# Performance work log

Measured on AMD Instinct MI355X. Metric: run time of the kernel, lower is better.

Reference implementation:

```python
import jax, jax.numpy as jnp
import numpy as np

B = 1024      # batchsz
T = 80        # max_review_len
E = 100       # embedding_len
U = 256       # units
V = 10000     # total_words


def _lstm_cell(x, c, h, wf, bf, wi, bi, wc, bc, wo, bo):
    # Faithful to LSTMlayer.call: four separate concat+matmul+bias gates.
    hx = jnp.concatenate([h, x], axis=1)          # [B, U + sec_dim]
    gf = jax.nn.sigmoid(hx @ wf + bf)             # forget gate
    gi = jax.nn.sigmoid(hx @ wi + bi)             # input gate (gr / wr1)
    ct = jnp.tanh(hx @ wc + bc)                   # candidate (wr2)
    c_new = gf * c + gi * ct
    go = jax.nn.sigmoid(hx @ wo + bo)             # output gate
    h_new = go * jnp.tanh(c_new)
    return c_new, h_new


def setup_inputs() -> dict:
    key = jax.random.key(0)
    ks = jax.random.split(key, 21)
    inp = {"tokens": jax.random.randint(ks[0], (B, T), 0, V, dtype=jnp.int32)}
    inp["emb"] = jax.random.normal(ks[1], (V, E), dtype=jnp.float32) * 0.1
    # Layer 1: sec_dim = E; Layer 2: sec_dim = U. stddev=0.1 matches init_weights.
    names = ["wf1", "wi1", "wc1", "wo1", "wf2", "wi2", "wc2", "wo2"]
    dims = [U + E] * 4 + [U + U] * 4
    for i, (n, d) in enumerate(zip(names, dims)):
        inp[n] = jax.random.normal(ks[2 + i], (d, U), dtype=jnp.float32) * 0.1
        inp["b" + n[1:]] = jnp.zeros((U,), dtype=jnp.float32)
    inp["w_out"] = jax.random.normal(ks[10], (U, 1), dtype=jnp.float32) * 0.1
    inp["b_out"] = jnp.zeros((1,), dtype=jnp.float32)
    return inp


def reference(tokens, emb, wf1, bf1, wi1, bi1, wc1, bc1, wo1, bo1,
              wf2, bf2, wi2, bi2, wc2, bc2, wo2, bo2, w_out, b_out):
    x = emb[tokens]                               # [B, T, E]
    init = (jnp.zeros((B, U), x.dtype), jnp.zeros((B, U), x.dtype),
            jnp.zeros((B, U), x.dtype), jnp.zeros((B, U), x.dtype))

    def step(carry, xt):
        c1, h1, c2, h2 = carry
        c1, h1 = _lstm_cell(xt, c1, h1, wf1, bf1, wi1, bi1, wc1, bc1, wo1, bo1)
        c2, h2 = _lstm_cell(h1, c2, h2, wf2, bf2, wi2, bi2, wc2, bc2, wo2, bo2)
        return (c1, h1, c2, h2), None

    carry, _ = jax.lax.scan(step, init, jnp.swapaxes(x, 0, 1))  # scan over T
    h2_last = carry[3]                            # [B, U]
    return jax.nn.sigmoid(h2_last @ w_out + b_out)  # [B, 1]
```

## Files before the change

### kernel.cpp

```cpp
#include <hip/hip_runtime.h>

typedef unsigned short u16;
typedef unsigned int uint;

using f32x4 = __attribute__((ext_vector_type(4))) float;
using bf16x8 = __attribute__((ext_vector_type(8))) __bf16;
using u32x4 = __attribute__((ext_vector_type(4))) uint;

static __device__ __forceinline__ bf16x8 as_bf16x8(uint4 u) {
    union { uint4 a; bf16x8 b; } c; c.a = u; return c.b;
}
static __device__ __forceinline__ bf16x8 as_bf16x8v(u32x4 u) {
    union { u32x4 a; bf16x8 b; } c; c.a = u; return c.b;
}
static __device__ __forceinline__ float bf2f(u16 h) {
    union { uint u; float f; } c; c.u = ((uint)h) << 16; return c.f;
}
static __device__ __forceinline__ u16 f2bf(float f) {
    union { float f; uint u; } c; c.f = f;
    uint u = c.u;
    return (u16)((u + 0x7fffu + ((u >> 16) & 1u)) >> 16);
}
static __device__ __forceinline__ float fast_sigmoid(float x) {
    x = fminf(30.f, fmaxf(-30.f, x));
    return __builtin_amdgcn_rcpf(1.0f + __builtin_amdgcn_exp2f(x * -1.44269504f));
}
static __device__ __forceinline__ float fast_tanh(float x) {
    x = fminf(15.f, fmaxf(-15.f, x));
    return 1.0f - 2.0f * __builtin_amdgcn_rcpf(1.0f + __builtin_amdgcn_exp2f(x * 2.88539008f));
}

static __device__ __forceinline__ u32x4 load_b128_sc0(const u16* p) {
    u32x4 r;
    asm volatile("global_load_dwordx4 %0, %1, off sc0" : "=v"(r) : "v"(p) : "memory");
    return r;
}
static __device__ __forceinline__ void wait_vm0_fence_sched() {
    asm volatile("s_waitcnt vmcnt(0)" ::: "memory");
    __builtin_amdgcn_sched_barrier(0);
}

static __device__ __forceinline__ float vext(f32x4 v, int i) {
    float r = v[0];
    r = (i == 1) ? v[1] : r;
    r = (i == 2) ? v[2] : r;
    r = (i == 3) ? v[3] : r;
    return r;
}
static __device__ __forceinline__ float sel4(float a0, float a1, float a2, float a3, int i) {
    float r = a0;
    r = (i == 1) ? a1 : r;
    r = (i == 2) ? a2 : r;
    r = (i == 3) ? a3 : r;
    return r;
}

static __device__ __forceinline__ int detect_fp32(const uint* w, int nwords) {
    int hits = 0;
    for (int i = 0; i < nwords; ++i) { uint e = (w[i] >> 7) & 0xffu; hits += (e >= 0x80u); }
    return hits > (nwords >> 3);
}
static __device__ __forceinline__ u16 load_bf(const void* p, int i, int fp32) {
    return fp32 ? f2bf(((const float*)p)[i]) : ((const u16*)p)[i];
}

__global__ void pack_w(const void* wf, const void* wi, const void* wc, const void* wo,
                       const void* bbf, const void* bbi, const void* bbc, const void* bbo,
                       u16* __restrict__ wp, u16* __restrict__ bp, int K, int KSTEPS) {
    __shared__ int sfp;
    if (threadIdx.x == 0) sfp = detect_fp32((const uint*)wf, 256);
    __syncthreads();
    const int fp32 = sfp;
    int w = blockIdx.x / KSTEPS, ks = blockIdx.x % KSTEPS;
    int nt = threadIdx.x >> 6, lane = threadIdx.x & 63;
    int c16 = lane & 15, q = lane >> 4;
    int n = w * 64 + nt * 16 + c16;
    int u = n >> 2, g = n & 3;
    const void* W = (g == 0) ? wf : (g == 1) ? wi : (g == 2) ? wc : wo;
    union { u16 v[8]; uint4 u4; } tmp;
#pragma unroll
    for (int j = 0; j < 8; ++j) {
        int k = ks * 32 + q * 8 + j;
        tmp.v[j] = (k < K) ? load_bf(W, k * 256 + u, fp32) : (u16)0;
    }
    *(uint4*)(wp + ((w * KSTEPS + ks) * 4 + nt) * 512 + lane * 8) = tmp.u4;
    if (ks == 0 && threadIdx.x < 64) {
        int n2 = w * 64 + threadIdx.x;
        int g2 = n2 & 3;
        const void* B = (g2 == 0) ? bbf : (g2 == 1) ? bbi : (g2 == 2) ? bbc : bbo;
        bp[n2] = load_bf(B, n2 >> 2, fp32);
    }
}

__global__ void pack_misc(const void* emb, const void* w_out, const void* b_out,
                          u16* __restrict__ embp, u16* __restrict__ wob,
                          u16* __restrict__ bob, uint* __restrict__ hzero) {
    __shared__ int sfp;
    if (threadIdx.x == 0) sfp = detect_fp32((const uint*)emb, 256);
    __syncthreads();
    const int fp32 = sfp;
    int gid = blockIdx.x * blockDim.x + threadIdx.x;
    int stride = gridDim.x * blockDim.x;
    for (int i = gid; i < 1000000; i += stride)
        embp[i] = load_bf(emb, i, fp32);
    for (int i = gid; i < 526336; i += stride) hzero[i] = 0;
    if (blockIdx.x == 0) {
        __shared__ int sfp2;
        if (threadIdx.x == 0) sfp2 = detect_fp32((const uint*)w_out, 128);
        __syncthreads();
        if (threadIdx.x < 256) wob[threadIdx.x] = load_bf(w_out, threadIdx.x, sfp2);
        if (threadIdx.x == 0) bob[0] = load_bf(b_out, 0, sfp2);
    }
}

static __device__ __forceinline__ void wv_wait(uint* grp, uint phase, int lane) {
    const uint* fp = grp + (lane & 15);
    uint* cnt = grp + 32;
    int k = 0;
    while (true) {
        uint v;
        asm volatile("global_load_dword %0, %1, off sc0\n\t"
                     "s_waitcnt vmcnt(0)"
                     : "=v"(v) : "v"(fp) : "memory");
        if (__all((int)(v >= phase))) break;
        __builtin_amdgcn_s_sleep(2);
        if (((++k) & 7) == 0 &&
            __hip_atomic_load(cnt, __ATOMIC_RELAXED,
                              __HIP_MEMORY_SCOPE_AGENT) >= 16u * phase)
            break;
    }
}

static __device__ __forceinline__ void wv_arrive(uint* ldsc_ch, uint* grp, int g,
                                                 uint phase, int lane) {
    asm volatile("s_waitcnt vmcnt(0)" ::: "memory");
    if (lane == 0) {
        uint old = __hip_atomic_fetch_add(ldsc_ch, 1u, __ATOMIC_RELAXED,
                                          __HIP_MEMORY_SCOPE_WORKGROUP);
        if (old == 8u * phase - 1u) {
            uint* slot = grp + g;
            asm volatile("global_store_dword %0, %1, off sc0"
                         :: "v"(slot), "v"(phase) : "memory");
            __hip_atomic_fetch_add(grp + 32, 1u, __ATOMIC_RELAXED,
                                   __HIP_MEMORY_SCOPE_AGENT);
        }
    }
}

#define CSLAB 16384

__global__ void __launch_bounds__(1024, 1)
lstm_kernel(const int* __restrict__ tokens, const u16* __restrict__ embp,
            const u16* __restrict__ wp1, const u16* __restrict__ b1p,
            const u16* __restrict__ wp2, const u16* __restrict__ b2p,
            const u16* __restrict__ wob, const u16* __restrict__ bob,
            u16* __restrict__ h1g, u16* __restrict__ h2g,
            uint* __restrict__ flags, float* __restrict__ out) {
    __shared__ __align__(16) u16 w1s[12 * 4 * 512];
    __shared__ __align__(16) u16 w2s[16 * 4 * 512];
    __shared__ uint ldsc[2];
    __shared__ __align__(16) float outscr[1024];

    const int tid = threadIdx.x;
    const int bid = blockIdx.x;
    const int r2 = bid & 7;
    const int g = bid >> 3;
    const int lane = tid & 63;
    const int wv = tid >> 6;
    const int half = wv >> 3;
    const int w8 = wv & 7;
    const int nt = w8 & 3;
    const int mb = (w8 >> 2) * 2;
    const int c16 = lane & 15, q = lane >> 4;

    const int b = lane & 3;
    const int ulz = nt * 4 + ((lane & 15) >> 2);
    const int gunit = g * 16 + ulz;

    {
        const uint4* s1 = (const uint4*)(wp1 + g * (12 * 4 * 512));
        uint4* d1 = (uint4*)w1s;
        for (int i = tid; i < 3072; i += 1024) d1[i] = s1[i];
        const uint4* s2 = (const uint4*)(wp2 + g * (16 * 4 * 512));
        uint4* d2 = (uint4*)w2s;
        for (int i = tid; i < 4096; i += 1024) d2[i] = s2[i];
        if (tid < 2) ldsc[tid] = 0u;
    }
    ushort4 bl1 = *(const ushort4*)(b1p + gunit * 4);
    ushort4 bl2 = *(const ushort4*)(b2p + gunit * 4);
    const float b1f = bf2f(bl1.x), b1i = bf2f(bl1.y), b1c = bf2f(bl1.z), b1o = bf2f(bl1.w);
    const float b2f = bf2f(bl2.x), b2i = bf2f(bl2.y), b2c = bf2f(bl2.z), b2o = bf2f(bl2.w);
    float c1a = 0.f, c1b = 0.f, c2a = 0.f, c2b = 0.f;
    uint* fg = flags + (half * 8 + r2) * 64;
    uint* lc = &ldsc[half];
    __syncthreads();

    const u16* bp1 = w1s + nt * 512 + lane * 8;
    const u16* bp2 = w2s + nt * 512 + lane * 8;

    ushort4 xlo[4], xhi[4];
#define LOAD_X(m, t)                                                           \
    {                                                                          \
        int row = r2 * 128 + half * 64 + (m) * 16 + c16;                       \
        int tok = tokens[row * 80 + (t)];                                      \
        const u16* xb = embp + tok * 100 + q * 8;                              \
        _Pragma("unroll")                                                      \
        for (int k2 = 0; k2 < 4; ++k2) {                                       \
            xlo[k2] = *(const ushort4*)(xb + k2 * 32);                         \
            xhi[k2] = *(const ushort4*)(xb + k2 * 32 + 4);                     \
        }                                                                      \
    }
#define XFRAG(k2) ({ union { ushort4 a[2]; bf16x8 v; } xu;                     \
                     xu.a[0] = xlo[k2]; xu.a[1] = xhi[k2]; xu.v; })

#define GATES(accv, B0, B1, B2, B3, cref, hout)                                \
    {                                                                          \
        float v0 = vext(accv, b);                                              \
        float v1 = __shfl_xor(vext(accv, b ^ 1), 1, 64);                       \
        float v2 = __shfl_xor(vext(accv, b ^ 2), 2, 64);                       \
        float v3 = __shfl_xor(vext(accv, b ^ 3), 3, 64);                       \
        float zf = sel4(v0, v1, v2, v3, b);                                    \
        float zi = sel4(v0, v1, v2, v3, b ^ 1);                                \
        float zc = sel4(v0, v1, v2, v3, b ^ 2);                                \
        float zo = sel4(v0, v1, v2, v3, b ^ 3);                                \
        float gf = fast_sigmoid(zf + B0);                                      \
        float gi = fast_sigmoid(zi + B1);                                      \
        float gc = fast_tanh(zc + B2);                                         \
        float go = fast_sigmoid(zo + B3);                                      \
        float cn = gf * cref + gi * gc;                                        \
        cref = cn;                                                             \
        hout = f2bf(go * fast_tanh(cn));                                       \
    }

#define MSUB(m, acc1, c1ref, c2ref, p2r, p1r, p2w, p1w)                        \
    {                                                                          \
        const int loffm = (q >> 1) * 1024 + ((m) * 16 + c16) * 16 + (q & 1) * 8; \
        const int hidxm = g * 1024 + ((m) * 16 + q * 4 + b) * 16 + ulz;        \
        const u16* h2b = h2g + (((p2r) * 2 + half) * 8 + r2) * CSLAB + loffm;  \
        const u16* h1b = h1g + (((p1r) * 2 + half) * 8 + r2) * CSLAB + loffm;  \
        u32x4 ag2[8], ag1[8];                                                  \
        _Pragma("unroll")                                                      \
        for (int ks = 0; ks < 8; ++ks) ag2[ks] = load_b128_sc0(h2b + ks * 2048); \
        _Pragma("unroll")                                                      \
        for (int ks = 0; ks < 8; ++ks) ag1[ks] = load_b128_sc0(h1b + ks * 2048); \
        wait_vm0_fence_sched();                                                \
        f32x4 acc2 = (f32x4){0.f, 0.f, 0.f, 0.f};                              \
        _Pragma("unroll")                                                      \
        for (int ks = 0; ks < 8; ++ks)                                         \
            acc2 = __builtin_amdgcn_mfma_f32_16x16x32_bf16(                    \
                as_bf16x8v(ag2[ks]), as_bf16x8(*(const uint4*)(bp2 + ks * 2048)), acc2, 0, 0, 0); \
        _Pragma("unroll")                                                      \
        for (int ks = 0; ks < 8; ++ks)                                         \
            acc2 = __builtin_amdgcn_mfma_f32_16x16x32_bf16(                    \
                as_bf16x8v(ag1[ks]), as_bf16x8(*(const uint4*)(bp2 + (8 + ks) * 2048)), acc2, 0, 0, 0); \
        _Pragma("unroll")                                                      \
        for (int ks = 0; ks < 8; ++ks)                                         \
            acc1 = __builtin_amdgcn_mfma_f32_16x16x32_bf16(                    \
                as_bf16x8v(ag1[ks]), as_bf16x8(*(const uint4*)(bp1 + ks * 2048)), acc1, 0, 0, 0); \
        u16 h2o, h1o;                                                          \
        GATES(acc2, b2f, b2i, b2c, b2o, c2ref, h2o);                           \
        GATES(acc1, b1f, b1i, b1c, b1o, c1ref, h1o);                           \
        h2g[(((p2w) * 2 + half) * 8 + r2) * CSLAB + hidxm] = h2o;              \
        h1g[(((p1w) * 2 + half) * 8 + r2) * CSLAB + hidxm] = h1o;              \
    }

    {
        LOAD_X(mb, 0);
        f32x4 acc = (f32x4){0.f, 0.f, 0.f, 0.f};
#pragma unroll
        for (int k2 = 0; k2 < 4; ++k2)
            acc = __builtin_amdgcn_mfma_f32_16x16x32_bf16(
                XFRAG(k2), as_bf16x8(*(const uint4*)(bp1 + (8 + k2) * 2048)), acc, 0, 0, 0);
        u16 h1o;
        GATES(acc, b1f, b1i, b1c, b1o, c1a, h1o);
        h1g[((0 * 2 + half) * 8 + r2) * CSLAB + g * 1024 + (mb * 16 + q * 4 + b) * 16 + ulz] = h1o;
        LOAD_X(mb + 1, 0);
        f32x4 accB = (f32x4){0.f, 0.f, 0.f, 0.f};
#pragma unroll
        for (int k2 = 0; k2 < 4; ++k2)
            accB = __builtin_amdgcn_mfma_f32_16x16x32_bf16(
                XFRAG(k2), as_bf16x8(*(const uint4*)(bp1 + (8 + k2) * 2048)), accB, 0, 0, 0);
        u16 h1oB;
        GATES(accB, b1f, b1i, b1c, b1o, c1b, h1oB);
        h1g[((0 * 2 + half) * 8 + r2) * CSLAB + g * 1024 + ((mb + 1) * 16 + q * 4 + b) * 16 + ulz] = h1oB;
        wv_arrive(lc, fg, g, 1u, lane);
    }

#pragma unroll 1
    for (int i = 0; i < 79; ++i) {
        const int p_h2r = (i + 1) & 1, p_h1r = i & 1;
        const int p_h2w = i & 1, p_h1w = (i + 1) & 1;

        LOAD_X(mb, i + 1);
        f32x4 acc1a = (f32x4){0.f, 0.f, 0.f, 0.f};
#pragma unroll
        for (int k2 = 0; k2 < 4; ++k2)
            acc1a = __builtin_amdgcn_mfma_f32_16x16x32_bf16(
                XFRAG(k2), as_bf16x8(*(const uint4*)(bp1 + (8 + k2) * 2048)), acc1a, 0, 0, 0);
        LOAD_X(mb + 1, i + 1);
        f32x4 acc1b = (f32x4){0.f, 0.f, 0.f, 0.f};
#pragma unroll
        for (int k2 = 0; k2 < 4; ++k2)
            acc1b = __builtin_amdgcn_mfma_f32_16x16x32_bf16(
                XFRAG(k2), as_bf16x8(*(const uint4*)(bp1 + (8 + k2) * 2048)), acc1b, 0, 0, 0);

        wv_wait(fg, (uint)(i + 1), lane);

        __builtin_amdgcn_s_setprio(1);
        MSUB(mb, acc1a, c1a, c2a, p_h2r, p_h1r, p_h2w, p_h1w);
        MSUB(mb + 1, acc1b, c1b, c2b, p_h2r, p_h1r, p_h2w, p_h1w);
        __builtin_amdgcn_s_setprio(0);

        wv_arrive(lc, fg, g, (uint)(i + 2), lane);
    }

    {
        wv_wait(fg, 80u, lane);
#pragma unroll 1
        for (int s = 0; s < 2; ++s) {
            const int m = mb + s;
            const int loffm = (q >> 1) * 1024 + (m * 16 + c16) * 16 + (q & 1) * 8;
            const int hidxm = g * 1024 + (m * 16 + q * 4 + b) * 16 + ulz;
            const u16* h2b = h2g + ((0 * 2 + half) * 8 + r2) * CSLAB + loffm;
            const u16* h1b = h1g + ((1 * 2 + half) * 8 + r2) * CSLAB + loffm;
            u32x4 ag2[8], ag1[8];
#pragma unroll
            for (int ks = 0; ks < 8; ++ks) ag2[ks] = load_b128_sc0(h2b + ks * 2048);
#pragma unroll
            for (int ks = 0; ks < 8; ++ks) ag1[ks] = load_b128_sc0(h1b + ks * 2048);
            wait_vm0_fence_sched();
            f32x4 acc2 = (f32x4){0.f, 0.f, 0.f, 0.f};
#pragma unroll
            for (int ks = 0; ks < 8; ++ks)
                acc2 = __builtin_amdgcn_mfma_f32_16x16x32_bf16(
                    as_bf16x8v(ag2[ks]), as_bf16x8(*(const uint4*)(bp2 + ks * 2048)), acc2, 0, 0, 0);
#pragma unroll
            for (int ks = 0; ks < 8; ++ks)
                acc2 = __builtin_amdgcn_mfma_f32_16x16x32_bf16(
                    as_bf16x8v(ag1[ks]), as_bf16x8(*(const uint4*)(bp2 + (8 + ks) * 2048)), acc2, 0, 0, 0);
            u16 h2o;
            if (s == 0) { GATES(acc2, b2f, b2i, b2c, b2o, c2a, h2o); }
            else        { GATES(acc2, b2f, b2i, b2c, b2o, c2b, h2o); }
            h2g[((1 * 2 + half) * 8 + r2) * CSLAB + hidxm] = h2o;
        }
        wv_arrive(lc, fg, g, 81u, lane);
        wv_wait(fg, 81u, lane);
    }
    __syncthreads();

    if (g == 0) {
#pragma unroll 1
        for (int ch = 0; ch < 2; ++ch) {
            const u16* base = h2g + ((1 * 2 + ch) * 8 + r2) * CSLAB;
            int rr = tid >> 4, s = tid & 15;
            const u16* hp = base + s * 1024 + rr * 16;
            u32x4 hv0 = load_b128_sc0(hp);
            u32x4 hv1 = load_b128_sc0(hp + 8);
            wait_vm0_fence_sched();
            const u16* wq = wob + s * 16;
            union { u32x4 v[2]; u16 h[16]; } hu; hu.v[0] = hv0; hu.v[1] = hv1;
            float dot = 0.f;
#pragma unroll
            for (int k = 0; k < 16; ++k) dot += bf2f(hu.h[k]) * bf2f(wq[k]);
            __syncthreads();
            outscr[rr * 16 + s] = dot;
            __syncthreads();
            if (tid < 64) {
                float ssum = 0.f;
                for (int k = 0; k < 16; ++k) ssum += outscr[tid * 16 + k];
                out[r2 * 128 + ch * 64 + tid] = fast_sigmoid(ssum + bf2f(bob[0]));
            }
        }
    }
}

extern "C" void kernel_launch(void* const* d_in, const int* in_sizes, int n_in,
                              void* d_out, int out_size, void* d_ws, size_t ws_size,
                              hipStream_t stream) {
    const int* tokens = (const int*)d_in[0];
    const void* emb = d_in[1];
    const void* wf1 = d_in[2];  const void* bf1_ = d_in[3];
    const void* wi1 = d_in[4];  const void* bi1_ = d_in[5];
    const void* wc1 = d_in[6];  const void* bc1_ = d_in[7];
    const void* wo1 = d_in[8];  const void* bo1_ = d_in[9];
    const void* wf2 = d_in[10]; const void* bf2_ = d_in[11];
    const void* wi2 = d_in[12]; const void* bi2_ = d_in[13];
    const void* wc2 = d_in[14]; const void* bc2_ = d_in[15];
    const void* wo2 = d_in[16]; const void* bo2_ = d_in[17];
    const void* w_out = d_in[18];
    const void* b_out = d_in[19];

    u16* wp1 = (u16*)d_ws;
    u16* wp2 = wp1 + 16 * 12 * 4 * 512;
    u16* b1p = wp2 + 16 * 16 * 4 * 512;
    u16* b2p = b1p + 1024;
    u16* wob = b2p + 1024;
    u16* bob = wob + 256;
    u16* embp = bob + 8;
    u16* h1g = embp + 1000000;
    u16* h2g = h1g + 524288;
    uint* flags = (uint*)(h2g + 524288);

    pack_w<<<dim3(16 * 12), dim3(256), 0, stream>>>(wf1, wi1, wc1, wo1, bf1_, bi1_, bc1_, bo1_,
                                                    wp1, b1p, 356, 12);
    pack_w<<<dim3(16 * 16), dim3(256), 0, stream>>>(wf2, wi2, wc2, wo2, bf2_, bi2_, bc2_, bo2_,
                                                    wp2, b2p, 512, 16);
    pack_misc<<<dim3(512), dim3(256), 0, stream>>>(emb, w_out, b_out, embp, wob, bob, (uint*)h1g);
    lstm_kernel<<<dim3(128), dim3(1024), 0, stream>>>(tokens, embp, wp1, b1p, wp2, b2p,
                                                      wob, bob, h1g, h2g, flags, (float*)d_out);
}
```

Measured before the change: 782.0 us.

## Replace global barrier wait with per-fragment readiness polling and pipelined K-loop

Instead of waiting for all producer groups to finish a timestep before loading hidden state, each wave polls per-group flags and waits only for the K-slice it needs next. It starts at a staggered slice offset (gp) so consumers fan out across producers. Loads for the next slice are double-buffered against the MFMAs of the current one, and the two M-subtiles are interleaved. This aims to overlap cross-block synchronization latency with compute, at the cost of more flag polling traffic and a more complex ordering that depends on flag semantics.

```diff
diff --git a/kernel.cpp b/kernel.cpp
--- a/kernel.cpp
+++ b/kernel.cpp
@@ -165,6 +165,7 @@
     const int bid = blockIdx.x;
     const int r2 = bid & 7;
     const int g = bid >> 3;
+    const int gp = g >> 1;
     const int lane = tid & 63;
     const int wv = tid >> 6;
     const int half = wv >> 3;
@@ -232,36 +233,57 @@
         hout = f2bf(go * fast_tanh(cn));                                       \
     }
 
-#define MSUB(m, acc1, c1ref, c2ref, p2r, p1r, p2w, p1w)                        \
+#define FRAG_WAIT(ksp, ph)                                                     \
+    if (((rmask >> (2 * (ksp))) & 3u) != 3u) {                                 \
+        const uint* fpp = fg + (lane & 15);                                    \
+        uint* cntp = fg + 32;                                                  \
+        int kk = 0;                                                            \
+        while (true) {                                                         \
+            uint v;                                                            \
+            asm volatile("global_load_dword %0, %1, off sc0\n\t"               \
+                         "s_waitcnt vmcnt(0)"                                  \
+                         : "=v"(v) : "v"(fpp) : "memory");                     \
+            unsigned long long bl = __ballot((int)(v >= (ph)));                \
+            rmask = (uint)(bl & 0xffffull);                                    \
+            if (((rmask >> (2 * (ksp))) & 3u) == 3u) break;                    \
+            __builtin_amdgcn_s_sleep(1);                                       \
+            if (((++kk) & 15) == 0 &&                                          \
+                __hip_atomic_load(cntp, __ATOMIC_RELAXED,                      \
+                                  __HIP_MEMORY_SCOPE_AGENT) >= 16u * (ph)) {   \
+                rmask = 0xffffu;                                               \
+                break;                                                         \
+            }                                                                  \
+        }                                                                      \
+    }
+
+#define FRAG_STEP(J)                                                           \
     {                                                                          \
-        const int loffm = (q >> 1) * 1024 + ((m) * 16 + c16) * 16 + (q & 1) * 8; \
-        const int hidxm = g * 1024 + ((m) * 16 + q * 4 + b) * 16 + ulz;        \
-        const u16* h2b = h2g + (((p2r) * 2 + half) * 8 + r2) * CSLAB + loffm;  \
-        const u16* h1b = h1g + (((p1r) * 2 + half) * 8 + r2) * CSLAB + loffm;  \
-        u32x4 ag2[8], ag1[8];                                                  \
-        _Pragma("unroll")                                                      \
-        for (int ks = 0; ks < 8; ++ks) ag2[ks] = load_b128_sc0(h2b + ks * 2048); \
-        _Pragma("unroll")                                                      \
-        for (int ks = 0; ks < 8; ++ks) ag1[ks] = load_b128_sc0(h1b + ks * 2048); \
-        wait_vm0_fence_sched();                                                \
-        f32x4 acc2 = (f32x4){0.f, 0.f, 0.f, 0.f};                              \
-        _Pragma("unroll")                                                      \
-        for (int ks = 0; ks < 8; ++ks)                                         \
-            acc2 = __builtin_amdgcn_mfma_f32_16x16x32_bf16(                    \
-                as_bf16x8v(ag2[ks]), as_bf16x8(*(const uint4*)(bp2 + ks * 2048)), acc2, 0, 0, 0); \
-        _Pragma("unroll")                                                      \
-        for (int ks = 0; ks < 8; ++ks)                                         \
-            acc2 = __builtin_amdgcn_mfma_f32_16x16x32_bf16(                    \
-                as_bf16x8v(ag1[ks]), as_bf16x8(*(const uint4*)(bp2 + (8 + ks) * 2048)), acc2, 0, 0, 0); \
-        _Pragma("unroll")                                                      \
-        for (int ks = 0; ks < 8; ++ks)                                         \
-            acc1 = __builtin_amdgcn_mfma_f32_16x16x32_bf16(                    \
-                as_bf16x8v(ag1[ks]), as_bf16x8(*(const uint4*)(bp1 + ks * 2048)), acc1, 0, 0, 0); \
-        u16 h2o, h1o;                                                          \
-        GATES(acc2, b2f, b2i, b2c, b2o, c2ref, h2o);                           \
-        GATES(acc1, b1f, b1i, b1c, b1o, c1ref, h1o);                           \
-        h2g[(((p2w) * 2 + half) * 8 + r2) * CSLAB + hidxm] = h2o;              \
-        h1g[(((p1w) * 2 + half) * 8 + r2) * CSLAB + hidxm] = h1o;              \
+        u32x4 n2a = f2a, n1a = f1a, n2b = f2b, n1b = f1b;                      \
+        if ((J) < 7) {                                                         \
+            int kspn = (gp + (J) + 1) & 7;                                     \
+            FRAG_WAIT(kspn, phase);                                            \
+            const u16* h2fn = h2base + kspn * 2048;                            \
+            const u16* h1fn = h1base + kspn * 2048;                            \
+            n2a = load_b128_sc0(h2fn + loffA);                                 \
+            n1a = load_b128_sc0(h1fn + loffA);                                 \
+            n2b = load_b128_sc0(h2fn + loffB);                                 \
+            n1b = load_b128_sc0(h1fn + loffB);                                 \
+            asm volatile("s_waitcnt vmcnt(4)" ::: "memory");                   \
+        } else {                                                               \
+            asm volatile("s_waitcnt vmcnt(0)" ::: "memory");                   \
+        }                                                                      \
+        __builtin_amdgcn_sched_barrier(0);                                     \
+        int kspc = (gp + (J)) & 7;                                             \
+        const uint4 w2lo = *(const uint4*)(bp2 + kspc * 2048);                 \
+        const uint4 w2hi = *(const uint4*)(bp2 + (8 + kspc) * 2048);           \
+        const uint4 w1lo = *(const uint4*)(bp1 + kspc * 2048);                 \
+        acc2a = __builtin_amdgcn_mfma_f32_16x16x32_bf16(as_bf16x8v(f2a), as_bf16x8(w2lo), acc2a, 0, 0, 0); \
+        acc1a = __builtin_amdgcn_mfma_f32_16x16x32_bf16(as_bf16x8v(f1a), as_bf16x8(w1lo), acc1a, 0, 0, 0); \
+        acc2a = __builtin_amdgcn_mfma_f32_16x16x32_bf16(as_bf16x8v(f1a), as_bf16x8(w2hi), acc2a, 0, 0, 0); \
+        acc2b = __builtin_amdgcn_mfma_f32_16x16x32_bf16(as_bf16x8v(f2b), as_bf16x8(w2lo), acc2b, 0, 0, 0); \
+        acc1b = __builtin_amdgcn_mfma_f32_16x16x32_bf16(as_bf16x8v(f1b), as_bf16x8(w1lo), acc1b, 0, 0, 0); \
+        acc2b = __builtin_amdgcn_mfma_f32_16x16x32_bf16(as_bf16x8v(f1b), as_bf16x8(w2hi), acc2b, 0, 0, 0); \
+        f2a = n2a; f1a = n1a; f2b = n2b; f1b = n1b;                            \
     }
 
     {
@@ -304,11 +326,38 @@
             acc1b = __builtin_amdgcn_mfma_f32_16x16x32_bf16(
                 XFRAG(k2), as_bf16x8(*(const uint4*)(bp1 + (8 + k2) * 2048)), acc1b, 0, 0, 0);
 
-        wv_wait(fg, (uint)(i + 1), lane);
+        const uint phase = (uint)(i + 1);
+        const u16* h2base = h2g + ((p_h2r * 2 + half) * 8 + r2) * CSLAB;
+        const u16* h1base = h1g + ((p_h1r * 2 + half) * 8 + r2) * CSLAB;
+        const int loffA = (q >> 1) * 1024 + (mb * 16 + c16) * 16 + (q & 1) * 8;
+        const int loffB = loffA + 256;
+        f32x4 acc2a = (f32x4){0.f, 0.f, 0.f, 0.f};
+        f32x4 acc2b = (f32x4){0.f, 0.f, 0.f, 0.f};
+        uint rmask = 0u;
+
+        FRAG_WAIT(gp, phase);
+        const u16* h2f0 = h2base + gp * 2048;
+        const u16* h1f0 = h1base + gp * 2048;
+        u32x4 f2a = load_b128_sc0(h2f0 + loffA);
+        u32x4 f1a = load_b128_sc0(h1f0 + loffA);
+        u32x4 f2b = load_b128_sc0(h2f0 + loffB);
+        u32x4 f1b = load_b128_sc0(h1f0 + loffB);
 
         __builtin_amdgcn_s_setprio(1);
-        MSUB(mb, acc1a, c1a, c2a, p_h2r, p_h1r, p_h2w, p_h1w);
-        MSUB(mb + 1, acc1b, c1b, c2b, p_h2r, p_h1r, p_h2w, p_h1w);
+        FRAG_STEP(0) FRAG_STEP(1) FRAG_STEP(2) FRAG_STEP(3)
+        FRAG_STEP(4) FRAG_STEP(5) FRAG_STEP(6) FRAG_STEP(7)
+
+        u16 h2oA, h1oA, h2oB, h1oB;
+        GATES(acc2a, b2f, b2i, b2c, b2o, c2a, h2oA);
+        GATES(acc1a, b1f, b1i, b1c, b1o, c1a, h1oA);
+        GATES(acc2b, b2f, b2i, b2c, b2o, c2b, h2oB);
+        GATES(acc1b, b1f, b1i, b1c, b1o, c1b, h1oB);
+        const int hidxA = g * 1024 + (mb * 16 + q * 4 + b) * 16 + ulz;
+        const int hidxB = hidxA + 256;
+        h2g[((p_h2w * 2 + half) * 8 + r2) * CSLAB + hidxA] = h2oA;
+        h1g[((p_h1w * 2 + half) * 8 + r2) * CSLAB + hidxA] = h1oA;
+        h2g[((p_h2w * 2 + half) * 8 + r2) * CSLAB + hidxB] = h2oB;
+        h1g[((p_h1w * 2 + half) * 8 + r2) * CSLAB + hidxB] = h1oB;
         __builtin_amdgcn_s_setprio(0);
 
         wv_arrive(lc, fg, g, (uint)(i + 2), lane);
```

New measurement: 848.8 us. 1.09x slower.
